# Kernel optimization log

Hardware: AMD Instinct MI355X
Metric: run time of the kernel (lower is better)

Reference implementation:

```python
import jax, jax.numpy as jnp
import numpy as np

N = 4096        # nodes
E = 131072      # edges (avg degree 32)
IN = 256        # in_channels
OUT = 64        # out_channels per head
HEADS = 4


def setup_inputs() -> dict:
    key = jax.random.key(0)
    k1, k2, k3, k4 = jax.random.split(key, 4)
    h = jax.random.normal(k1, (N, IN), dtype=jnp.float32)
    edge_index = jax.random.randint(k2, (2, E), 0, N, dtype=jnp.int64)
    # Linear weights, one per head: [HEADS, OUT, IN] (torch Linear layout)
    W = jax.random.normal(k3, (HEADS, OUT, IN), dtype=jnp.float32) * (1.0 / np.sqrt(IN))
    # attention vector a: xavier_uniform with gain=1.414, shape [2*OUT, 1]
    limit = 1.414 * np.sqrt(6.0 / (2 * OUT + 1))
    a = jax.random.uniform(k4, (HEADS, 2 * OUT, 1), dtype=jnp.float32, minval=-limit, maxval=limit)
    return {"h": h, "edge_index": edge_index, "W": W, "a": a}


def _head(h, row, col, Wf, af):
    # Wh = Linear(h): [N, OUT]
    Wh = h @ Wf.T
    # e = leakyrelu(cat(Wh[row], Wh[col]) @ a) == Wh[row]@a1 + Wh[col]@a2
    a1 = af[:OUT, 0]
    a2 = af[OUT:, 0]
    e = jax.nn.leaky_relu(Wh[row] @ a1 + Wh[col] @ a2, negative_slope=0.2)
    # dense N x N scatter (faithful to original: non-edges contribute exp(0))
    alpha = jnp.zeros((h.shape[0], h.shape[0]), dtype=h.dtype).at[row, col].set(e)
    alpha = jax.nn.softmax(alpha, axis=1)
    h_prime = alpha @ Wh  # [N, OUT]
    return h_prime, alpha


def reference(h, edge_index, W, a):
    row, col = edge_index[0], edge_index[1]
    # vmap over heads: h_prime [HEADS, N, OUT], attn [HEADS, N, N]
    h_prime, attn = jax.vmap(lambda Wf, af: _head(h, row, col, Wf, af))(W, a)
    # concat heads along features, then relu
    out = jax.nn.relu(jnp.transpose(h_prime, (1, 0, 2)).reshape(h.shape[0], HEADS * OUT))
    return out, attn.mean(axis=0)
```

## Files before the change

### kernel.cpp

```cpp
#include <hip/hip_runtime.h>

#define N_NODES 4096
#define E_EDGES 131072
#define IN_F    256
#define OUT_F   64
#define HEADS   4
#define HC      256
#define CAP     128

typedef float v4f __attribute__((ext_vector_type(4)));
typedef short v8s __attribute__((ext_vector_type(8)));
typedef float v4acc __attribute__((ext_vector_type(4)));

__device__ __forceinline__ unsigned short bf16_rn(float x) {
    unsigned u = __builtin_bit_cast(unsigned, x);
    unsigned r = (u + 0x7FFFu + ((u >> 16) & 1u)) >> 16;
    return (unsigned short)r;
}
__device__ __forceinline__ float bf16_to_f(unsigned short b) {
    unsigned u = ((unsigned)b) << 16;
    return __builtin_bit_cast(float, u);
}

__global__ void k_init_prep(const float* __restrict__ h, const float* __restrict__ W,
                            unsigned short* __restrict__ h_hi, unsigned short* __restrict__ h_lo,
                            unsigned short* __restrict__ W_hi, unsigned short* __restrict__ W_lo,
                            int* __restrict__ rowcnt, float* __restrict__ S) {
    const int i = blockIdx.x * blockDim.x + threadIdx.x;
    if (i < N_NODES) rowcnt[i] = 0;
    if (i < HC)      S[i] = 0.f;
    const int HN = N_NODES * IN_F;
    const int WN = HC * IN_F;
    if (i < HN) {
        float x = h[i];
        unsigned short hi = bf16_rn(x);
        h_hi[i] = hi;
        h_lo[i] = bf16_rn(x - bf16_to_f(hi));
    } else if (i < HN + WN) {
        int j = i - HN;
        float x = W[j];
        unsigned short hi = bf16_rn(x);
        W_hi[j] = hi;
        W_lo[j] = bf16_rn(x - bf16_to_f(hi));
    }
}

__global__ __launch_bounds__(256) void k_linear_mfma(
        const unsigned short* __restrict__ h_hi, const unsigned short* __restrict__ h_lo,
        const unsigned short* __restrict__ W_hi, const unsigned short* __restrict__ W_lo,
        const float* __restrict__ a,
        float* __restrict__ Wh, float* __restrict__ s1, float* __restrict__ s2,
        float* __restrict__ S) {
    const int t = threadIdx.x;
    const int wave = t >> 6, lane = t & 63;
    const int n16 = lane & 15, quad = lane >> 4;
    const int node0 = blockIdx.x * 16;
    const int ch0 = wave * 64;
    const int head = wave;

    v4acc acc[4];
#pragma unroll
    for (int nt = 0; nt < 4; ++nt) acc[nt] = (v4acc){0.f, 0.f, 0.f, 0.f};

    const int arow = (node0 + n16) * IN_F;
#pragma unroll
    for (int s = 0; s < 8; ++s) {
        const int k0 = s * 32 + quad * 8;
        v8s Ah = *(const v8s*)(h_hi + arow + k0);
        v8s Al = *(const v8s*)(h_lo + arow + k0);
#pragma unroll
        for (int nt = 0; nt < 4; ++nt) {
            const int ch = ch0 + nt * 16 + n16;
            v8s Bh = *(const v8s*)(W_hi + ch * IN_F + k0);
            v8s Bl = *(const v8s*)(W_lo + ch * IN_F + k0);
            acc[nt] = __builtin_amdgcn_mfma_f32_16x16x32_bf16(Ah, Bh, acc[nt], 0, 0, 0);
            acc[nt] = __builtin_amdgcn_mfma_f32_16x16x32_bf16(Ah, Bl, acc[nt], 0, 0, 0);
            acc[nt] = __builtin_amdgcn_mfma_f32_16x16x32_bf16(Al, Bh, acc[nt], 0, 0, 0);
        }
    }

#pragma unroll
    for (int nt = 0; nt < 4; ++nt) {
        const int ch = ch0 + nt * 16 + n16;
#pragma unroll
        for (int r = 0; r < 4; ++r)
            Wh[(size_t)(node0 + quad * 4 + r) * HC + ch] = acc[nt][r];
    }

    float a1v[4], a2v[4];
#pragma unroll
    for (int nt = 0; nt < 4; ++nt) {
        a1v[nt] = a[head * 2 * OUT_F + nt * 16 + n16];
        a2v[nt] = a[head * 2 * OUT_F + OUT_F + nt * 16 + n16];
    }
#pragma unroll
    for (int r = 0; r < 4; ++r) {
        float p1 = acc[0][r] * a1v[0] + acc[1][r] * a1v[1] + acc[2][r] * a1v[2] + acc[3][r] * a1v[3];
        float p2 = acc[0][r] * a2v[0] + acc[1][r] * a2v[1] + acc[2][r] * a2v[2] + acc[3][r] * a2v[3];
#pragma unroll
        for (int o = 1; o < 16; o <<= 1) {
            p1 += __shfl_xor(p1, o, 64);
            p2 += __shfl_xor(p2, o, 64);
        }
        if (n16 == 0) {
            const int node = node0 + quad * 4 + r;
            s1[node * HEADS + head] = p1;
            s2[node * HEADS + head] = p2;
        }
    }

#pragma unroll
    for (int nt = 0; nt < 4; ++nt) {
        float cp = acc[nt][0] + acc[nt][1] + acc[nt][2] + acc[nt][3];
        cp += __shfl_xor(cp, 16, 64);
        cp += __shfl_xor(cp, 32, 64);
        if (quad == 0) atomicAdd(&S[ch0 + nt * 16 + n16], cp);
    }
}

__global__ void k_append(const int* __restrict__ rows, int* __restrict__ rowcnt,
                         int* __restrict__ slots) {
    const int k = blockIdx.x * blockDim.x + threadIdx.x;
    const int r = rows[k];
    const int pos = atomicAdd(&rowcnt[r], 1);
    if (pos < CAP) slots[r * CAP + pos] = k;
}

__global__ __launch_bounds__(256) void k_row_mega(
        const int* __restrict__ rowcnt, const int* __restrict__ slots,
        const int* __restrict__ cols,
        const float* __restrict__ s1, const float* __restrict__ s2,
        const float* __restrict__ S, const float* __restrict__ Wh,
        float* __restrict__ out0, float* __restrict__ attn) {
    __shared__ float rowbuf[N_NODES];
    __shared__ float eh[HEADS][CAP];
    __shared__ float wgt[HEADS][CAP];
    __shared__ int   kk[CAP];
    __shared__ int   cc[CAP];
    __shared__ int   wflag[CAP];
    __shared__ float mh[HEADS], dh[HEADS], bh[HEADS];
    __shared__ int   nw_sh;

    const int i = blockIdx.x;
    const int t = threadIdx.x, head = t >> 6, lane = t & 63;
    int cnt = rowcnt[i];
    if (cnt > CAP) cnt = CAP;
    if (t == 0) nw_sh = 0;

    const float4 s1r = *(const float4*)(s1 + i * HEADS);

    for (int q = t; q < cnt; q += 256) {
        const int k = slots[i * CAP + q];
        const int c = cols[k];
        kk[q] = k; cc[q] = c;
        const float4 s2c = *(const float4*)(s2 + c * HEADS);
        float x;
        x = s1r.x + s2c.x; eh[0][q] = (x > 0.f) ? x : 0.2f * x;
        x = s1r.y + s2c.y; eh[1][q] = (x > 0.f) ? x : 0.2f * x;
        x = s1r.z + s2c.z; eh[2][q] = (x > 0.f) ? x : 0.2f * x;
        x = s1r.w + s2c.w; eh[3][q] = (x > 0.f) ? x : 0.2f * x;
    }
    __syncthreads();

    int mycount = 0;
    for (int q = t; q < cnt; q += 256) {
        const int c = cc[q], k = kk[q];
        int win = 1;
        for (int q2 = 0; q2 < cnt; ++q2)
            if (cc[q2] == c && kk[q2] > k) { win = 0; break; }
        wflag[q] = win;
        mycount += win;
    }
#pragma unroll
    for (int o = 32; o > 0; o >>= 1) mycount += __shfl_xor(mycount, o, 64);
    if (lane == 0 && mycount) atomicAdd(&nw_sh, mycount);
    __syncthreads();
    const int nw = nw_sh;

    float emax = -1e30f;
    for (int q = lane; q < cnt; q += 64)
        if (wflag[q]) emax = fmaxf(emax, eh[head][q]);
#pragma unroll
    for (int o = 32; o > 0; o >>= 1) emax = fmaxf(emax, __shfl_xor(emax, o, 64));
    const float m = fmaxf(emax, 0.f);

    float ssum = 0.f;
    for (int q = lane; q < cnt; q += 64)
        if (wflag[q]) ssum += __expf(eh[head][q] - m);
#pragma unroll
    for (int o = 32; o > 0; o >>= 1) ssum += __shfl_xor(ssum, o, 64);

    if (lane == 0) {
        const float denom = ssum + (float)(N_NODES - nw) * __expf(-m);
        mh[head] = m;
        dh[head] = denom;
        bh[head] = __expf(-m) / denom;
    }
    __syncthreads();
    const float bsum = 0.25f * (bh[0] + bh[1] + bh[2] + bh[3]);

    {
        float4 v4 = make_float4(bsum, bsum, bsum, bsum);
        float4* rb4 = (float4*)rowbuf;
        for (int j = t; j < N_NODES / 4; j += 256) rb4[j] = v4;
    }
    __syncthreads();

    for (int q = t; q < cnt; q += 256) {
        const float w0 = __expf(eh[0][q] - mh[0]) / dh[0];
        const float w1 = __expf(eh[1][q] - mh[1]) / dh[1];
        const float w2 = __expf(eh[2][q] - mh[2]) / dh[2];
        const float w3 = __expf(eh[3][q] - mh[3]) / dh[3];
        wgt[0][q] = w0; wgt[1][q] = w1; wgt[2][q] = w2; wgt[3][q] = w3;
        if (wflag[q]) rowbuf[cc[q]] = 0.25f * (w0 + w1 + w2 + w3);
    }
    __syncthreads();

    {
        const v4f* src = (const v4f*)rowbuf;
        v4f* dst = (v4f*)(attn + (size_t)i * N_NODES);
        for (int j = t; j < N_NODES / 4; j += 256)
            __builtin_nontemporal_store(src[j], &dst[j]);
    }

    const float b_ = bh[head];
    float acc = b_ * S[t];
    for (int q = 0; q < cnt; ++q) {
        if (wflag[q])
            acc += (wgt[head][q] - b_) * Wh[(size_t)cc[q] * HC + t];
    }
    out0[(size_t)i * HC + t] = fmaxf(acc, 0.f);
}

extern "C" void kernel_launch(void* const* d_in, const int* in_sizes, int n_in,
                              void* d_out, int out_size, void* d_ws, size_t ws_size,
                              hipStream_t stream) {
    const float* h  = (const float*)d_in[0];
    const int*   ei = (const int*)d_in[1];
    const float* W  = (const float*)d_in[2];
    const float* a  = (const float*)d_in[3];
    const int* rows = ei;
    const int* cols = ei + E_EDGES;

    float* out0 = (float*)d_out;
    float* attn = out0 + (size_t)N_NODES * HC;

    char* p = (char*)d_ws;
    auto carve = [&](size_t bytes) { char* q = p; p += (bytes + 255) & ~(size_t)255; return q; };
    float* Wh      = (float*)carve(sizeof(float) * (size_t)N_NODES * HC);
    float* s1      = (float*)carve(sizeof(float) * N_NODES * HEADS);
    float* s2      = (float*)carve(sizeof(float) * N_NODES * HEADS);
    float* S       = (float*)carve(sizeof(float) * HC);
    int*   rowcnt  = (int*)carve(sizeof(int) * N_NODES);
    int*   slots   = (int*)carve(sizeof(int) * (size_t)N_NODES * CAP);
    unsigned short* h_hi = (unsigned short*)carve(sizeof(short) * (size_t)N_NODES * IN_F);
    unsigned short* h_lo = (unsigned short*)carve(sizeof(short) * (size_t)N_NODES * IN_F);
    unsigned short* W_hi = (unsigned short*)carve(sizeof(short) * HC * IN_F);
    unsigned short* W_lo = (unsigned short*)carve(sizeof(short) * HC * IN_F);

    k_init_prep<<<(N_NODES * IN_F + HC * IN_F) / 256, 256, 0, stream>>>(
        h, W, h_hi, h_lo, W_hi, W_lo, rowcnt, S);
    k_linear_mfma<<<N_NODES / 16, 256, 0, stream>>>(h_hi, h_lo, W_hi, W_lo, a, Wh, s1, s2, S);
    k_append<<<E_EDGES / 256, 256, 0, stream>>>(rows, rowcnt, slots);
    k_row_mega<<<N_NODES, 256, 0, stream>>>(rowcnt, slots, cols, s1, s2, S, Wh, out0, attn);
}
```

Baseline: 166.9 us.

## Split row kernel into stats, dense attn fill, and sparse scatter passes

```diff
diff --git a/kernel.cpp b/kernel.cpp
--- a/kernel.cpp
+++ b/kernel.cpp
@@ -126,18 +126,19 @@
     if (pos < CAP) slots[r * CAP + pos] = k;
 }
 
-__global__ __launch_bounds__(256) void k_row_mega(
+__global__ __launch_bounds__(256) void k_stats(
         const int* __restrict__ rowcnt, const int* __restrict__ slots,
         const int* __restrict__ cols,
         const float* __restrict__ s1, const float* __restrict__ s2,
         const float* __restrict__ S, const float* __restrict__ Wh,
-        float* __restrict__ out0, float* __restrict__ attn) {
-    __shared__ float rowbuf[N_NODES];
+        float* __restrict__ out0, float* __restrict__ bsum,
+        int* __restrict__ gnw, int* __restrict__ gcol, float* __restrict__ gws) {
     __shared__ float eh[HEADS][CAP];
-    __shared__ float wgt[HEADS][CAP];
     __shared__ int   kk[CAP];
     __shared__ int   cc[CAP];
-    __shared__ int   wflag[CAP];
+    __shared__ int   wcol[CAP];
+    __shared__ float weh[HEADS][CAP];
+    __shared__ float wgt[HEADS][CAP];
     __shared__ float mh[HEADS], dh[HEADS], bh[HEADS];
     __shared__ int   nw_sh;
 
@@ -162,31 +163,29 @@
     }
     __syncthreads();
 
-    int mycount = 0;
     for (int q = t; q < cnt; q += 256) {
         const int c = cc[q], k = kk[q];
         int win = 1;
         for (int q2 = 0; q2 < cnt; ++q2)
             if (cc[q2] == c && kk[q2] > k) { win = 0; break; }
-        wflag[q] = win;
-        mycount += win;
-    }
-#pragma unroll
-    for (int o = 32; o > 0; o >>= 1) mycount += __shfl_xor(mycount, o, 64);
-    if (lane == 0 && mycount) atomicAdd(&nw_sh, mycount);
+        if (win) {
+            const int pos = atomicAdd(&nw_sh, 1);
+            wcol[pos] = c;
+            weh[0][pos] = eh[0][q]; weh[1][pos] = eh[1][q];
+            weh[2][pos] = eh[2][q]; weh[3][pos] = eh[3][q];
+        }
+    }
     __syncthreads();
     const int nw = nw_sh;
 
     float emax = -1e30f;
-    for (int q = lane; q < cnt; q += 64)
-        if (wflag[q]) emax = fmaxf(emax, eh[head][q]);
+    for (int q = lane; q < nw; q += 64) emax = fmaxf(emax, weh[head][q]);
 #pragma unroll
     for (int o = 32; o > 0; o >>= 1) emax = fmaxf(emax, __shfl_xor(emax, o, 64));
     const float m = fmaxf(emax, 0.f);
 
     float ssum = 0.f;
-    for (int q = lane; q < cnt; q += 64)
-        if (wflag[q]) ssum += __expf(eh[head][q] - m);
+    for (int q = lane; q < nw; q += 64) ssum += __expf(weh[head][q] - m);
 #pragma unroll
     for (int o = 32; o > 0; o >>= 1) ssum += __shfl_xor(ssum, o, 64);
 
@@ -197,39 +196,48 @@
         bh[head] = __expf(-m) / denom;
     }
     __syncthreads();
-    const float bsum = 0.25f * (bh[0] + bh[1] + bh[2] + bh[3]);
-
-    {
-        float4 v4 = make_float4(bsum, bsum, bsum, bsum);
-        float4* rb4 = (float4*)rowbuf;
-        for (int j = t; j < N_NODES / 4; j += 256) rb4[j] = v4;
-    }
-    __syncthreads();
-
-    for (int q = t; q < cnt; q += 256) {
-        const float w0 = __expf(eh[0][q] - mh[0]) / dh[0];
-        const float w1 = __expf(eh[1][q] - mh[1]) / dh[1];
-        const float w2 = __expf(eh[2][q] - mh[2]) / dh[2];
-        const float w3 = __expf(eh[3][q] - mh[3]) / dh[3];
+
+    for (int q = t; q < nw; q += 256) {
+        const float w0 = __expf(weh[0][q] - mh[0]) / dh[0];
+        const float w1 = __expf(weh[1][q] - mh[1]) / dh[1];
+        const float w2 = __expf(weh[2][q] - mh[2]) / dh[2];
+        const float w3 = __expf(weh[3][q] - mh[3]) / dh[3];
         wgt[0][q] = w0; wgt[1][q] = w1; wgt[2][q] = w2; wgt[3][q] = w3;
-        if (wflag[q]) rowbuf[cc[q]] = 0.25f * (w0 + w1 + w2 + w3);
-    }
-    __syncthreads();
-
-    {
-        const v4f* src = (const v4f*)rowbuf;
-        v4f* dst = (v4f*)(attn + (size_t)i * N_NODES);
-        for (int j = t; j < N_NODES / 4; j += 256)
-            __builtin_nontemporal_store(src[j], &dst[j]);
-    }
+        gcol[i * CAP + q] = wcol[q];
+        gws[i * CAP + q]  = 0.25f * (w0 + w1 + w2 + w3);
+    }
+    if (t == 0) {
+        gnw[i] = nw;
+        bsum[i] = 0.25f * (bh[0] + bh[1] + bh[2] + bh[3]);
+    }
+    __syncthreads();
 
     const float b_ = bh[head];
     float acc = b_ * S[t];
-    for (int q = 0; q < cnt; ++q) {
-        if (wflag[q])
-            acc += (wgt[head][q] - b_) * Wh[(size_t)cc[q] * HC + t];
-    }
+    for (int q = 0; q < nw; ++q)
+        acc += (wgt[head][q] - b_) * Wh[(size_t)wcol[q] * HC + t];
     out0[(size_t)i * HC + t] = fmaxf(acc, 0.f);
+}
+
+__global__ __launch_bounds__(256) void k_attn_fill(const float* __restrict__ bsum,
+                                                   float* __restrict__ attn) {
+    const int i = blockIdx.x;
+    const float v = bsum[i];
+    const float4 v4 = make_float4(v, v, v, v);
+    float4* rowp = (float4*)(attn + (size_t)i * N_NODES);
+#pragma unroll
+    for (int rep = 0; rep < 4; ++rep)
+        rowp[rep * 256 + threadIdx.x] = v4;
+}
+
+__global__ __launch_bounds__(256) void k_attn_scatter(
+        const int* __restrict__ gnw, const int* __restrict__ gcol,
+        const float* __restrict__ gws, float* __restrict__ attn) {
+    const int wave = threadIdx.x >> 6, lane = threadIdx.x & 63;
+    const int i = blockIdx.x * 4 + wave;
+    const int nw = gnw[i];
+    for (int q = lane; q < nw; q += 64)
+        attn[(size_t)i * N_NODES + gcol[i * CAP + q]] = gws[i * CAP + q];
 }
 
 extern "C" void kernel_launch(void* const* d_in, const int* in_sizes, int n_in,
@@ -251,8 +259,12 @@
     float* s1      = (float*)carve(sizeof(float) * N_NODES * HEADS);
     float* s2      = (float*)carve(sizeof(float) * N_NODES * HEADS);
     float* S       = (float*)carve(sizeof(float) * HC);
+    float* bsum    = (float*)carve(sizeof(float) * N_NODES);
     int*   rowcnt  = (int*)carve(sizeof(int) * N_NODES);
     int*   slots   = (int*)carve(sizeof(int) * (size_t)N_NODES * CAP);
+    int*   gnw     = (int*)carve(sizeof(int) * N_NODES);
+    int*   gcol    = (int*)carve(sizeof(int) * (size_t)N_NODES * CAP);
+    float* gws     = (float*)carve(sizeof(float) * (size_t)N_NODES * CAP);
     unsigned short* h_hi = (unsigned short*)carve(sizeof(short) * (size_t)N_NODES * IN_F);
     unsigned short* h_lo = (unsigned short*)carve(sizeof(short) * (size_t)N_NODES * IN_F);
     unsigned short* W_hi = (unsigned short*)carve(sizeof(short) * HC * IN_F);
@@ -262,5 +274,8 @@
         h, W, h_hi, h_lo, W_hi, W_lo, rowcnt, S);
     k_linear_mfma<<<N_NODES / 16, 256, 0, stream>>>(h_hi, h_lo, W_hi, W_lo, a, Wh, s1, s2, S);
     k_append<<<E_EDGES / 256, 256, 0, stream>>>(rows, rowcnt, slots);
-    k_row_mega<<<N_NODES, 256, 0, stream>>>(rowcnt, slots, cols, s1, s2, S, Wh, out0, attn);
-}
+    k_stats<<<N_NODES, 256, 0, stream>>>(rowcnt, slots, cols, s1, s2, S, Wh,
+                                         out0, bsum, gnw, gcol, gws);
+    k_attn_fill<<<N_NODES, 256, 0, stream>>>(bsum, attn);
+    k_attn_scatter<<<N_NODES / 4, 256, 0, stream>>>(gnw, gcol, gws, attn);
+}
```

Result: faster. 153.2 us (-8.2%).
